# Kernel optimization log

Hardware: AMD Instinct MI355X
Metric: run time of the kernel (lower is better)

Reference implementation:

```python
import jax, jax.numpy as jnp
import numpy as np

B, CIN, COUT, CLEV = 1, 128, 128, 64
H, W = 48, 160            # height//2**scale, width//2**scale (scale=2)
MIN_D, MAX_D = 0.1, 100.0


def conv3x3(x, w, b, mode):
    x = jnp.pad(x, ((0, 0), (0, 0), (1, 1), (1, 1)), mode=mode)
    y = jax.lax.conv_general_dilated(x, w, (1, 1), 'VALID',
                                     dimension_numbers=('NCHW', 'OIHW', 'NCHW'))
    return y + b[None, :, None, None]


def head(x, w1, b1, w2, b2):  # gaussian head: conv -> GELU -> conv, replicate pad
    return conv3x3(jax.nn.gelu(conv3x3(x, w1, b1, 'edge')), w2, b2, 'edge')


def convblock(x, w, b):  # ConvBlock: 3x3 conv (reflect pad) + ELU
    return jax.nn.elu(conv3x3(x, w, b, 'reflect'))


def to_pts(t):  # [B,C,H,W] -> [B,HW,C]
    return t.transpose(0, 2, 3, 1).reshape(t.shape[0], -1, t.shape[1])


def quat_to_rot(q):  # [N,4] (w,x,y,z) -> [N,3,3]
    w, x, y, z = q[:, 0], q[:, 1], q[:, 2], q[:, 3]
    return jnp.stack([1 - 2 * (y * y + z * z), 2 * (x * y - w * z), 2 * (x * z + w * y),
                      2 * (x * y + w * z), 1 - 2 * (x * x + z * z), 2 * (y * z - w * x),
                      2 * (x * z - w * y), 2 * (y * z + w * x), 1 - 2 * (x * x + y * y)],
                     axis=-1).reshape(-1, 3, 3)


def rasterize_one(pos, rot, scl, opa, feat, K):
    # depth-sort gaussians front-to-back
    order = jnp.argsort(pos[:, 2])
    pos, rot, scl, opa, feat = pos[order], rot[order], scl[order], opa[order], feat[order]
    x, y, z = pos[:, 0], pos[:, 1], pos[:, 2]
    fx, fy, cx, cy = K[0, 0], K[1, 1], K[0, 2], K[1, 2]
    u, v = fx * x / z + cx, fy * y / z + cy
    # 3D covariance Sigma = R S S^T R^T, projected with perspective Jacobian J
    M = quat_to_rot(rot) * scl[:, None, :]
    Sig = jnp.einsum('nij,nkj->nik', M, M)
    zer = jnp.zeros_like(z)
    J = jnp.stack([fx / z, zer, -fx * x / z ** 2,
                   zer, fy / z, -fy * y / z ** 2], axis=-1).reshape(-1, 2, 3)
    cov = jnp.einsum('nij,njk,nlk->nil', J, Sig, J)
    a = cov[:, 0, 0] + 0.3  # low-pass blur as in 3DGS
    bq = cov[:, 0, 1]
    c = cov[:, 1, 1] + 0.3
    det = a * c - bq * bq
    A, Bc, C = c / det, -bq / det, a / det  # conic (inverse 2D covariance)
    gy, gx = jnp.meshgrid(jnp.arange(H, dtype=pos.dtype),
                          jnp.arange(W, dtype=pos.dtype), indexing='ij')
    dx = gx.reshape(-1)[:, None] - u[None, :]  # [P,N]
    dy = gy.reshape(-1)[:, None] - v[None, :]
    power = -0.5 * (A[None] * dx * dx + C[None] * dy * dy) - Bc[None] * dx * dy
    alpha = jnp.where(power <= 0.,
                      jnp.clip(opa[None, :, 0] * jnp.exp(jnp.minimum(power, 0.)), 0., 0.99),
                      0.)
    l1m = jnp.log1p(-alpha)
    logT = jnp.cumsum(l1m, axis=1) - l1m  # exclusive transmittance along sorted axis
    wgt = alpha * jnp.exp(logT)           # [P,N]
    return (wgt @ feat).T.reshape(-1, H, W)  # [C,H,W]


def forward(init_feature, disp_init, inv_K, K,
            rot_w1, rot_b1, rot_w2, rot_b2,
            scl_w1, scl_b1, scl_w2, scl_b2,
            opa_w1, opa_b1, opa_w2, opa_b2,
            fl_w1, fl_b1, fl_w2, fl_b2, fr_w, fr_b):
    bs = init_feature.shape[0]
    # disp_to_depth
    scaled = 1. / MAX_D + (1. / MIN_D - 1. / MAX_D) * disp_init
    depth = jnp.clip(1. / scaled, MIN_D, MAX_D)
    # backproject depth to a point cloud
    gy, gx = jnp.meshgrid(jnp.arange(H, dtype=depth.dtype),
                          jnp.arange(W, dtype=depth.dtype), indexing='ij')
    pix = jnp.stack([gx.ravel(), gy.ravel(), jnp.ones(H * W, depth.dtype)], 0)  # [3,HW]
    cam = jnp.einsum('bij,jn->bin', inv_K[:, :3, :3], pix) * depth.reshape(bs, 1, -1)
    position = cam.transpose(0, 2, 1)  # [B,N,3]
    rot = head(init_feature, rot_w1, rot_b1, rot_w2, rot_b2)
    rot = rot / jnp.maximum(jnp.linalg.norm(rot, axis=1, keepdims=True), 1e-12)
    rotation = to_pts(rot)  # [B,N,4]
    scale = to_pts(jnp.abs(head(init_feature, scl_w1, scl_b1, scl_w2, scl_b2)))
    opacity = to_pts(jax.nn.sigmoid(head(init_feature, opa_w1, opa_b1, opa_w2, opa_b2)))
    gs_feat = to_pts(convblock(convblock(init_feature, fl_w1, fl_b1), fl_w2, fl_b2))
    lev = jax.vmap(rasterize_one)(position, rotation, scale, opacity, gs_feat, K)
    return convblock(lev, fr_w, fr_b)


def setup_inputs() -> dict:
    key = jax.random.key(0)
    ks = jax.random.split(key, 16)
    p = lambda i, shape: jax.random.normal(ks[i], shape, jnp.float32) * 0.05
    Kmat = np.array([[0.58 * W, 0, 0.5 * W, 0],
                     [0, 1.92 * H, 0.5 * H, 0],
                     [0, 0, 1, 0],
                     [0, 0, 0, 1]], dtype=np.float32)
    inv_K = np.linalg.inv(Kmat)
    return {
        'init_feature': jax.random.normal(ks[0], (B, CIN, H, W), jnp.float32),
        'disp_init': jax.random.uniform(ks[1], (B, 1, H, W), jnp.float32, 0.01, 0.99),
        'inv_K': jnp.tile(jnp.asarray(inv_K)[None], (B, 1, 1)),
        'K': jnp.tile(jnp.asarray(Kmat)[None], (B, 1, 1)),
        'rot_w1': p(2, (8, CIN, 3, 3)), 'rot_b1': jnp.zeros(8),
        'rot_w2': p(3, (4, 8, 3, 3)), 'rot_b2': jnp.zeros(4),
        'scl_w1': p(4, (6, CIN, 3, 3)), 'scl_b1': jnp.zeros(6),
        'scl_w2': p(5, (3, 6, 3, 3)), 'scl_b2': jnp.zeros(3),
        'opa_w1': p(6, (2, CIN, 3, 3)), 'opa_b1': jnp.zeros(2),
        'opa_w2': p(7, (1, 2, 3, 3)), 'opa_b2': jnp.zeros(1),
        'fl_w1': p(8, (CIN, CIN, 3, 3)), 'fl_b1': jnp.zeros(CIN),
        'fl_w2': p(9, (CLEV, CIN, 3, 3)), 'fl_b2': jnp.zeros(CLEV),
        'fr_w': p(10, (COUT, CLEV, 3, 3)), 'fr_b': jnp.zeros(COUT),
    }


def reference(init_feature, disp_init, inv_K, K, rot_w1, rot_b1, rot_w2, rot_b2,
              scl_w1, scl_b1, scl_w2, scl_b2, opa_w1, opa_b1, opa_w2, opa_b2,
              fl_w1, fl_b1, fl_w2, fl_b2, fr_w, fr_b):
    return forward(init_feature, disp_init, inv_K, K, rot_w1, rot_b1, rot_w2, rot_b2,
                   scl_w1, scl_b1, scl_w2, scl_b2, opa_w1, opa_b1, opa_w2, opa_b2,
                   fl_w1, fl_b1, fl_w2, fl_b2, fr_w, fr_b)
```

## Files before the change

### kernel.cpp

```cpp
#include <hip/hip_runtime.h>
#include <hip/hip_bf16.h>
#include <math.h>

#define Hh 48
#define Ww 160
#define NP 7680

using bf16 = __hip_bfloat16;
typedef __attribute__((ext_vector_type(8))) short v8s;
typedef __attribute__((ext_vector_type(4))) float v4f;

__device__ __forceinline__ float bfdec(unsigned short u) {
  return __uint_as_float(((unsigned)u) << 16);
}
__device__ __forceinline__ unsigned short bfenc(float x) {
  bf16 b = __float2bfloat16(x);
  return *(unsigned short*)&b;
}
__device__ __forceinline__ float ldany(const void* p, size_t i, int isbf) {
  return isbf ? bfdec(((const unsigned short*)p)[i]) : ((const float*)p)[i];
}

__device__ __forceinline__ int mapidx(int i, int n, int mode) {
  if (mode == 0) return i < 0 ? 0 : (i >= n ? n - 1 : i);
  return i < 0 ? -i : (i >= n ? 2 * n - 2 - i : i);
}

__device__ __forceinline__ float eluf(float v) { return v > 0.f ? v : expm1f(v); }
__device__ __forceinline__ float geluf(float v) {
  float c = v + 0.044715f * v * v * v;
  return 0.5f * v * (1.f + tanhf(0.7978845608028654f * c));
}

__device__ __forceinline__ int sniff_local(const unsigned short* w, int* cnt) {
  int c = 0;
  for (int i = threadIdx.x; i < 2048; i += 256) {
    float a = fabsf(bfdec(w[i]));
    if (a > 1e-3f && a < 0.5f) c++;
  }
  cnt[threadIdx.x] = c;
  __syncthreads();
  for (int s = 128; s > 0; s >>= 1) {
    if (threadIdx.x < s) cnt[threadIdx.x] += cnt[threadIdx.x + s];
    __syncthreads();
  }
  int f = (cnt[0] > 1536) ? 1 : 0;
  __syncthreads();
  return f;
}

__global__ __launch_bounds__(256) void prep_all_k(int* __restrict__ flag,
    const void* __restrict__ xsrc, unsigned short* __restrict__ xb,
    const void* disp, const void* invK, const void* K, const void* rw2,
    const void* rb2, const void* sw2, const void* sb2, const void* ow2, const void* ob2,
    const void* rb1, const void* sb1, const void* ob1, const void* fb1, const void* fb2,
    const void* frb, const void* rot_w1, const void* scl_w1, const void* opa_w1,
    const void* fl_w1, const void* fl_w2, const void* fr_w,
    float* __restrict__ dispf, float* __restrict__ smallf, float* __restrict__ biasf,
    unsigned short* __restrict__ a_h1, unsigned short* __restrict__ a_fl1,
    unsigned short* __restrict__ a_fl2, unsigned short* __restrict__ a_fr) {
  __shared__ float tile[32][33];
  __shared__ int cnt[256];
  const int f = sniff_local((const unsigned short*)fl_w1, cnt);
  if (blockIdx.x == 0 && threadIdx.x == 0) flag[0] = f;
  if (blockIdx.x < 960) {
    const int bx = blockIdx.x;
    const int pb = (bx % 240) * 32, cb = (bx / 240) * 32;
#pragma unroll
    for (int pass = 0; pass < 4; pass++) {
      int ci = (threadIdx.x >> 5) + pass * 8, pl = threadIdx.x & 31;
      tile[ci][pl] = ldany(xsrc, (size_t)(cb + ci) * NP + pb + pl, f);
    }
    __syncthreads();
#pragma unroll
    for (int pass = 0; pass < 4; pass++) {
      int pl = (threadIdx.x >> 5) + pass * 8, ci = threadIdx.x & 31;
      xb[(size_t)(pb + pl) * 128 + cb + ci] = bfenc(tile[ci][pl]);
    }
    return;
  }
  int i = (blockIdx.x - 960) * 256 + threadIdx.x;
  if (i < 7680) { dispf[i] = ldany(disp, i, f); return; }
  i -= 7680;
  if (i < 508) {
    const void* src; int off;
    if (i < 16)       { src = invK; off = i; }
    else if (i < 32)  { src = K;    off = i - 16; }
    else if (i < 320) { src = rw2;  off = i - 32; }
    else if (i < 324) { src = rb2;  off = i - 320; }
    else if (i < 486) { src = sw2;  off = i - 324; }
    else if (i < 489) { src = sb2;  off = i - 486; }
    else if (i < 507) { src = ow2;  off = i - 489; }
    else              { src = ob2;  off = i - 507; }
    smallf[i] = ldany(src, off, f); return;
  }
  i -= 508;
  if (i < 336) {
    if (i < 8) biasf[i] = ldany(rb1, i, f);
    else if (i < 14) biasf[i] = ldany(sb1, i - 8, f);
    else if (i < 16) biasf[i] = ldany(ob1, i - 14, f);
    else if (i < 144) biasf[i] = ldany(fb1, i - 16, f);
    else if (i < 208) biasf[i] = ldany(fb2, i - 144, f);
    else biasf[i] = ldany(frb, i - 208, f);
    return;
  }
  i -= 336;
  if (i < 73728) {
    int co = i / 1152, rem = i - co * 1152;
    int t = rem >> 7, ci = rem & 127;
    float v = 0.f;
    if (co < 8) v = ldany(rot_w1, (size_t)co * 1152 + ci * 9 + t, f);
    else if (co < 14) v = ldany(scl_w1, (size_t)(co - 8) * 1152 + ci * 9 + t, f);
    else if (co < 16) v = ldany(opa_w1, (size_t)(co - 14) * 1152 + ci * 9 + t, f);
    a_h1[i] = bfenc(v); return;
  }
  i -= 73728;
  if (i < 147456) {
    int co = i / 1152, rem = i - co * 1152;
    int t = rem >> 7, ci = rem & 127;
    a_fl1[i] = bfenc(ldany(fl_w1, (size_t)co * 1152 + ci * 9 + t, f)); return;
  }
  i -= 147456;
  if (i < 73728) {
    int co = i / 1152, rem = i - co * 1152;
    int t = rem >> 7, ci = rem & 127;
    a_fl2[i] = bfenc(ldany(fl_w2, (size_t)co * 1152 + ci * 9 + t, f)); return;
  }
  i -= 73728;
  if (i < 73728) {
    int co = i / 576, rem = i - co * 576;
    int t = rem >> 6, ci = rem & 63;
    a_fr[i] = bfenc(ldany(fr_w, (size_t)co * 576 + ci * 9 + t, f));
    return;
  }
}

template<int OM, int PM, int ACT, bool GUARD, int KP, bool OPX>
__global__ __launch_bounds__(256) void gemm_conv4_k(const unsigned short* __restrict__ A,
    const unsigned short* __restrict__ X, const float* __restrict__ bias,
    void* __restrict__ out, const int* __restrict__ flag, int K, int glim) {
  __shared__ v8s As4[64][5];
  __shared__ v8s Bs4[64][5];
  __shared__ int off9s[64][9];
  const int tid = threadIdx.x;
  const int pxB = blockIdx.x * 64;
  const int coB = blockIdx.y * 64;
  if (tid < 64) {
    int p = pxB + tid;
    int h = p / Ww, w = p - h * Ww;
#pragma unroll
    for (int r = 0; r < 3; r++) {
      int hh = mapidx(h + r - 1, Hh, PM);
#pragma unroll
      for (int s = 0; s < 3; s++)
        off9s[tid][r * 3 + s] = hh * Ww + mapidx(w + s - 1, Ww, PM);
    }
  }
  const int lane = tid & 63, wv = tid >> 6;
  const int m16 = lane & 15, quad = lane >> 4;
  const int srow = tid >> 2, sg = tid & 3;
  v4f acc[4];
#pragma unroll
  for (int b = 0; b < 4; b++) acc[b] = (v4f){0.f, 0.f, 0.f, 0.f};
  __syncthreads();
  const int nIter = K >> 5;
  for (int it = 0; it < nIter; it++) {
    const int k0 = it << 5;
    {
      const unsigned short* ap = &A[(size_t)(coB + srow) * K + k0 + sg * 8];
      v8s av;
#pragma unroll
      for (int j = 0; j < 8; j++) av[j] = (short)ap[j];
      As4[srow][sg] = av;
    }
    {
      v8s bv;
      if (KP == 128) {
        int kk = k0 + sg * 8;
        int t = kk >> 7, c0 = kk & 127;
        const unsigned short* xp = &X[(size_t)off9s[srow][t] * 128 + c0];
#pragma unroll
        for (int j = 0; j < 8; j++) bv[j] = (short)xp[j];
      } else if (KP == 64) {
        int kk = k0 + sg * 8;
        int t = kk >> 6, c0 = kk & 63;
        const unsigned short* xp = &X[(size_t)off9s[srow][t] * 64 + c0];
#pragma unroll
        for (int j = 0; j < 8; j++) bv[j] = (short)xp[j];
      } else {
#pragma unroll
        for (int j = 0; j < 8; j++) {
          int k = k0 + sg * 8 + j;
          int ci = k / 9;
          int t = k - ci * 9;
          bv[j] = (short)X[(size_t)ci * NP + off9s[srow][t]];
        }
      }
      Bs4[srow][sg] = bv;
    }
    __syncthreads();
    v8s af = As4[wv * 16 + m16][quad];
    v8s bfr[4];
#pragma unroll
    for (int b = 0; b < 4; b++) bfr[b] = Bs4[b * 16 + m16][quad];
#pragma unroll
    for (int b = 0; b < 4; b++)
      acc[b] = __builtin_amdgcn_mfma_f32_16x16x32_bf16(af, bfr[b], acc[b], 0, 0, 0);
    __syncthreads();
  }
  const int obf = (OM == 2) ? *flag : (OM == 1);
#pragma unroll
  for (int b = 0; b < 4; b++) {
#pragma unroll
    for (int r = 0; r < 4; r++) {
      int co = coB + wv * 16 + quad * 4 + r;
      int px = pxB + b * 16 + m16;
      if (GUARD && co >= glim) continue;
      float bv = bias[GUARD ? (co & 15) : co];
      float v = acc[b][r] + bv;
      v = (ACT == 2) ? geluf(v) : eluf(v);
      size_t oi = OPX ? ((size_t)px * 128 + co) : ((size_t)co * NP + px);
      if (obf) ((unsigned short*)out)[oi] = bfenc(v);
      else ((float*)out)[oi] = v;
    }
  }
}

__global__ __launch_bounds__(256) void conv_fused1_k(
    const unsigned short* __restrict__ a_fl1, const unsigned short* __restrict__ a_h1,
    const unsigned short* __restrict__ X, const float* __restrict__ biasf,
    unsigned short* __restrict__ t1b, float* __restrict__ h1) {
  __shared__ v8s As4[64][5];
  __shared__ v8s Bs4[64][5];
  __shared__ int off9s[64][9];
  const int tid = threadIdx.x;
  const int zy = blockIdx.y;
  const bool ishead = (zy == 2);
  const int pm = ishead ? 0 : 1;
  const int pxB = blockIdx.x * 64;
  const int coB = ishead ? 0 : zy * 64;
  const unsigned short* A = ishead ? a_h1 : a_fl1;
  if (tid < 64) {
    int p = pxB + tid;
    int h = p / Ww, w = p - h * Ww;
#pragma unroll
    for (int r = 0; r < 3; r++) {
      int hh = mapidx(h + r - 1, Hh, pm);
#pragma unroll
      for (int s = 0; s < 3; s++)
        off9s[tid][r * 3 + s] = hh * Ww + mapidx(w + s - 1, Ww, pm);
    }
  }
  const int lane = tid & 63, wv = tid >> 6;
  const int m16 = lane & 15, quad = lane >> 4;
  const int srow = tid >> 2, sg = tid & 3;
  v4f acc[4];
#pragma unroll
  for (int b = 0; b < 4; b++) acc[b] = (v4f){0.f, 0.f, 0.f, 0.f};
  __syncthreads();
  for (int it = 0; it < 36; it++) {
    const int k0 = it << 5;
    {
      const unsigned short* ap = &A[(size_t)(coB + srow) * 1152 + k0 + sg * 8];
      v8s av;
#pragma unroll
      for (int j = 0; j < 8; j++) av[j] = (short)ap[j];
      As4[srow][sg] = av;
    }
    {
      int kk = k0 + sg * 8;
      int t = kk >> 7, c0 = kk & 127;
      const unsigned short* xp = &X[(size_t)off9s[srow][t] * 128 + c0];
      v8s bv;
#pragma unroll
      for (int j = 0; j < 8; j++) bv[j] = (short)xp[j];
      Bs4[srow][sg] = bv;
    }
    __syncthreads();
    v8s af = As4[wv * 16 + m16][quad];
    v8s bfr[4];
#pragma unroll
    for (int b = 0; b < 4; b++) bfr[b] = Bs4[b * 16 + m16][quad];
#pragma unroll
    for (int b = 0; b < 4; b++)
      acc[b] = __builtin_amdgcn_mfma_f32_16x16x32_bf16(af, bfr[b], acc[b], 0, 0, 0);
    __syncthreads();
  }
#pragma unroll
  for (int b = 0; b < 4; b++) {
#pragma unroll
    for (int r = 0; r < 4; r++) {
      int co = coB + wv * 16 + quad * 4 + r;
      int px = pxB + b * 16 + m16;
      if (ishead) {
        if (co < 16) h1[(size_t)co * NP + px] = geluf(acc[b][r] + biasf[co]);
      } else {
        t1b[(size_t)px * 128 + co] = bfenc(eluf(acc[b][r] + biasf[16 + co]));
      }
    }
  }
}

__global__ __launch_bounds__(256) void fl2_head2_k(
    const unsigned short* __restrict__ a_fl2, const unsigned short* __restrict__ t1b,
    const float* __restrict__ biasf, unsigned short* __restrict__ t2eb,
    const float* __restrict__ h1, const float* __restrict__ smallf,
    const float* __restrict__ dispf, float* __restrict__ params,
    float* __restrict__ zbuf) {
  __shared__ v8s As4[64][5];
  __shared__ v8s Bs4[64][5];
  __shared__ int off9s[64][9];
  const int tid = threadIdx.x;
  if (blockIdx.x < 120) {
    const int pxB = blockIdx.x * 64;
    if (tid < 64) {
      int p = pxB + tid;
      int h = p / Ww, w = p - h * Ww;
#pragma unroll
      for (int r = 0; r < 3; r++) {
        int hh = mapidx(h + r - 1, Hh, 1);
#pragma unroll
        for (int s = 0; s < 3; s++)
          off9s[tid][r * 3 + s] = hh * Ww + mapidx(w + s - 1, Ww, 1);
      }
    }
    const int lane = tid & 63, wv = tid >> 6;
    const int m16 = lane & 15, quad = lane >> 4;
    const int srow = tid >> 2, sg = tid & 3;
    v4f acc[4];
#pragma unroll
    for (int b = 0; b < 4; b++) acc[b] = (v4f){0.f, 0.f, 0.f, 0.f};
    __syncthreads();
    for (int it = 0; it < 36; it++) {
      const int k0 = it << 5;
      {
        const unsigned short* ap = &a_fl2[(size_t)srow * 1152 + k0 + sg * 8];
        v8s av;
#pragma unroll
        for (int j = 0; j < 8; j++) av[j] = (short)ap[j];
        As4[srow][sg] = av;
      }
      {
        int kk = k0 + sg * 8;
        int t = kk >> 7, c0 = kk & 127;
        const unsigned short* xp = &t1b[(size_t)off9s[srow][t] * 128 + c0];
        v8s bv;
#pragma unroll
        for (int j = 0; j < 8; j++) bv[j] = (short)xp[j];
        Bs4[srow][sg] = bv;
      }
      __syncthreads();
      v8s af = As4[wv * 16 + m16][quad];
      v8s bfr[4];
#pragma unroll
      for (int b = 0; b < 4; b++) bfr[b] = Bs4[b * 16 + m16][quad];
#pragma unroll
      for (int b = 0; b < 4; b++)
        acc[b] = __builtin_amdgcn_mfma_f32_16x16x32_bf16(af, bfr[b], acc[b], 0, 0, 0);
      __syncthreads();
    }
#pragma unroll
    for (int b = 0; b < 4; b++) {
#pragma unroll
      for (int r = 0; r < 4; r++) {
        int co = wv * 16 + quad * 4 + r;
        int px = pxB + b * 16 + m16;
        t2eb[(size_t)co * NP + px] = bfenc(eluf(acc[b][r] + biasf[144 + co]));
      }
    }
    return;
  }
  const float* invK = smallf;
  const float* Km   = smallf + 16;
  const float* rw2  = smallf + 32;
  const float* rb2  = smallf + 320;
  const float* sw2  = smallf + 324;
  const float* sb2  = smallf + 486;
  const float* ow2  = smallf + 489;
  const float* ob2  = smallf + 507;
  int p = (blockIdx.x - 120) * 256 + tid;
  if (p >= NP) return;
  int hh = p / Ww, ww = p - hh * Ww;
  float racc[4], sacc[3], oacc;
#pragma unroll
  for (int i = 0; i < 4; i++) racc[i] = rb2[i];
#pragma unroll
  for (int i = 0; i < 3; i++) sacc[i] = sb2[i];
  oacc = ob2[0];
  for (int ci = 0; ci < 16; ci++) {
    float t9[9];
#pragma unroll
    for (int r = 0; r < 3; r++) {
      int rr = mapidx(hh + r - 1, Hh, 0);
#pragma unroll
      for (int s = 0; s < 3; s++) {
        int cc = mapidx(ww + s - 1, Ww, 0);
        t9[r * 3 + s] = h1[(size_t)ci * NP + rr * Ww + cc];
      }
    }
    if (ci < 8) {
      for (int co = 0; co < 4; co++)
#pragma unroll
        for (int k = 0; k < 9; k++)
          racc[co] = fmaf(t9[k], rw2[(co * 8 + ci) * 9 + k], racc[co]);
    } else if (ci < 14) {
      int c2 = ci - 8;
      for (int co = 0; co < 3; co++)
#pragma unroll
        for (int k = 0; k < 9; k++)
          sacc[co] = fmaf(t9[k], sw2[(co * 6 + c2) * 9 + k], sacc[co]);
    } else {
      int c2 = ci - 14;
#pragma unroll
      for (int k = 0; k < 9; k++)
        oacc = fmaf(t9[k], ow2[c2 * 9 + k], oacc);
    }
  }
  float nq = sqrtf(racc[0]*racc[0] + racc[1]*racc[1] + racc[2]*racc[2] + racc[3]*racc[3]);
  nq = fmaxf(nq, 1e-12f);
  float qw = racc[0] / nq, qx = racc[1] / nq, qy = racc[2] / nq, qz = racc[3] / nq;
  float s0 = fabsf(sacc[0]), s1 = fabsf(sacc[1]), s2 = fabsf(sacc[2]);
  float opa = 1.f / (1.f + __expf(-oacc));
  float d = dispf[p];
  float scaled = 0.01f + 9.99f * d;
  float depth = fminf(fmaxf(1.f / scaled, 0.1f), 100.f);
  float M00 = invK[0], M01 = invK[1], M02 = invK[2];
  float M10 = invK[4], M11 = invK[5], M12 = invK[6];
  float M20 = invK[8], M21 = invK[9], M22 = invK[10];
  float gxf = (float)ww, gyf = (float)hh;
  float X = (M00 * gxf + M01 * gyf + M02) * depth;
  float Y = (M10 * gxf + M11 * gyf + M12) * depth;
  float Z = (M20 * gxf + M21 * gyf + M22) * depth;
  float fxk = Km[0], fyk = Km[5];
  float cxk = Km[2], cyk = Km[6];
  float u = fxk * X / Z + cxk;
  float v = fyk * Y / Z + cyk;
  float R00 = 1.f - 2.f*(qy*qy + qz*qz), R01 = 2.f*(qx*qy - qw*qz), R02 = 2.f*(qx*qz + qw*qy);
  float R10 = 2.f*(qx*qy + qw*qz), R11 = 1.f - 2.f*(qx*qx + qz*qz), R12 = 2.f*(qy*qz - qw*qx);
  float R20 = 2.f*(qx*qz - qw*qy), R21 = 2.f*(qy*qz + qw*qx), R22 = 1.f - 2.f*(qx*qx + qy*qy);
  float M0a = R00*s0, M0b = R01*s1, M0c = R02*s2;
  float M1a = R10*s0, M1b = R11*s1, M1c = R12*s2;
  float M2a = R20*s0, M2b = R21*s1, M2c = R22*s2;
  float S00 = M0a*M0a + M0b*M0b + M0c*M0c;
  float S01 = M0a*M1a + M0b*M1b + M0c*M1c;
  float S02 = M0a*M2a + M0b*M2b + M0c*M2c;
  float S11 = M1a*M1a + M1b*M1b + M1c*M1c;
  float S12 = M1a*M2a + M1b*M2b + M1c*M2c;
  float S22 = M2a*M2a + M2b*M2b + M2c*M2c;
  float iz = 1.f / Z;
  float j00 = fxk * iz, j02 = -fxk * X * iz * iz;
  float j11 = fyk * iz, j12 = -fyk * Y * iz * iz;
  float c00 = j00*j00*S00 + 2.f*j00*j02*S02 + j02*j02*S22 + 0.3f;
  float c01 = j00*j11*S01 + j00*j12*S02 + j02*j11*S12 + j02*j12*S22;
  float c11 = j11*j11*S11 + 2.f*j11*j12*S12 + j12*j12*S22 + 0.3f;
  float det = c00 * c11 - c01 * c01;
  float idet = 1.f / det;
  float* pr = params + (size_t)p * 8;
  pr[0] = u; pr[1] = v; pr[2] = c11 * idet; pr[3] = -c01 * idet;
  pr[4] = c00 * idet; pr[5] = opa; pr[6] = Z; pr[7] = 0.f;
  zbuf[p] = Z;
}

__global__ __launch_bounds__(256) void rank_sort_k(const float* __restrict__ zbuf,
                                                   int* __restrict__ ord) {
  __shared__ int part[32][9];
  const int g = threadIdx.x >> 3;
  const int seg = threadIdx.x & 7;
  const int i = blockIdx.x * 32 + g;
  const float zi = zbuf[i];
  const float4* zv = (const float4*)(zbuf + seg * 960);
  int cnt = 0;
  for (int t = 0; t < 240; t++) {
    float4 z4 = zv[t];
    int jb = seg * 960 + t * 4;
    cnt += (z4.x < zi || (z4.x == zi && jb + 0 < i)) ? 1 : 0;
    cnt += (z4.y < zi || (z4.y == zi && jb + 1 < i)) ? 1 : 0;
    cnt += (z4.z < zi || (z4.z == zi && jb + 2 < i)) ? 1 : 0;
    cnt += (z4.w < zi || (z4.w == zi && jb + 3 < i)) ? 1 : 0;
  }
  part[g][seg] = cnt;
  __syncthreads();
  if (seg == 0) {
    int c = part[g][0] + part[g][1] + part[g][2] + part[g][3]
          + part[g][4] + part[g][5] + part[g][6] + part[g][7];
    ord[c] = i;
  }
}

__global__ __launch_bounds__(64) void raster_seq_k(const int* __restrict__ ord,
    const float* __restrict__ params, const unsigned short* __restrict__ t2eb,
    unsigned short* __restrict__ levb) {
  __shared__ unsigned int Wl[64][17];
  __shared__ int ords[32];
  const int lane = threadIdx.x;
  const int m16 = lane & 15, quad = lane >> 4;
  const int pxB = blockIdx.x * 64;
  const int mypx = pxB + lane;
  const float px = (float)(mypx % Ww), py = (float)(mypx / Ww);
  float T = 1.f;
  v4f acc[4][4];
#pragma unroll
  for (int a = 0; a < 4; a++)
#pragma unroll
    for (int b = 0; b < 4; b++) acc[a][b] = (v4f){0.f, 0.f, 0.f, 0.f};
  for (int sub = 0; sub < NP / 32; sub++) {
    const int g0 = sub * 32;
    if (lane < 32) ords[lane] = ord[g0 + lane];
    __syncthreads();
    int myord[8];
#pragma unroll
    for (int j = 0; j < 8; j++) myord[j] = ords[quad * 8 + j];
    float al[32];
#pragma unroll
    for (int j = 0; j < 32; j++) {
      const float* pp = params + ((size_t)ords[j] << 3);
      float4 pa = *(const float4*)pp;
      float4 pb = *(const float4*)(pp + 4);
      float dx = px - pa.x, dy = py - pa.y;
      float power = -0.5f * (pa.z * dx * dx + pb.x * dy * dy) - pa.w * dx * dy;
      al[j] = fminf(pb.y * __expf(power), 0.99f);
    }
#pragma unroll
    for (int jj = 0; jj < 16; jj++) {
      float w0 = al[2 * jj] * T;     T *= 1.f - al[2 * jj];
      float w1 = al[2 * jj + 1] * T; T *= 1.f - al[2 * jj + 1];
      Wl[lane][jj] = (unsigned)bfenc(w0) | ((unsigned)bfenc(w1) << 16);
    }
    v8s af[4], bfr[4];
#pragma unroll
    for (int a = 0; a < 4; a++) {
      unsigned d0 = Wl[a * 16 + m16][quad * 4 + 0];
      unsigned d1 = Wl[a * 16 + m16][quad * 4 + 1];
      unsigned d2 = Wl[a * 16 + m16][quad * 4 + 2];
      unsigned d3 = Wl[a * 16 + m16][quad * 4 + 3];
      v8s t;
      t[0] = (short)(d0 & 0xffff); t[1] = (short)(d0 >> 16);
      t[2] = (short)(d1 & 0xffff); t[3] = (short)(d1 >> 16);
      t[4] = (short)(d2 & 0xffff); t[5] = (short)(d2 >> 16);
      t[6] = (short)(d3 & 0xffff); t[7] = (short)(d3 >> 16);
      af[a] = t;
    }
#pragma unroll
    for (int b = 0; b < 4; b++) {
      const unsigned short* fp = &t2eb[(size_t)(b * 16 + m16) * NP];
      v8s t;
#pragma unroll
      for (int j = 0; j < 8; j++) t[j] = (short)fp[myord[j]];
      bfr[b] = t;
    }
#pragma unroll
    for (int a = 0; a < 4; a++)
#pragma unroll
      for (int b = 0; b < 4; b++)
        acc[a][b] = __builtin_amdgcn_mfma_f32_16x16x32_bf16(af[a], bfr[b], acc[a][b], 0, 0, 0);
    if (__all(T < 1e-7f)) break;
    __syncthreads();
  }
#pragma unroll
  for (int a = 0; a < 4; a++) {
#pragma unroll
    for (int b = 0; b < 4; b++) {
#pragma unroll
      for (int r = 0; r < 4; r++) {
        levb[(size_t)(pxB + a * 16 + quad * 4 + r) * 64 + b * 16 + m16] =
            bfenc(acc[a][b][r]);
      }
    }
  }
}

extern "C" void kernel_launch(void* const* d_in, const int* in_sizes, int n_in,
                              void* d_out, int out_size, void* d_ws, size_t ws_size,
                              hipStream_t stream) {
  (void)in_sizes; (void)n_in; (void)out_size; (void)ws_size;
  const void* init_feature = d_in[0];
  const void* disp   = d_in[1];
  const void* invK   = d_in[2];
  const void* Km     = d_in[3];
  const void* rot_w1 = d_in[4];
  const void* rot_b1 = d_in[5];
  const void* rot_w2 = d_in[6];
  const void* rot_b2 = d_in[7];
  const void* scl_w1 = d_in[8];
  const void* scl_b1 = d_in[9];
  const void* scl_w2 = d_in[10];
  const void* scl_b2 = d_in[11];
  const void* opa_w1 = d_in[12];
  const void* opa_b1 = d_in[13];
  const void* opa_w2 = d_in[14];
  const void* opa_b2 = d_in[15];
  const void* fl_w1  = d_in[16];
  const void* fl_b1  = d_in[17];
  const void* fl_w2  = d_in[18];
  const void* fl_b2  = d_in[19];
  const void* fr_w   = d_in[20];
  const void* fr_b   = d_in[21];

  float* wsf = (float*)d_ws;
  int*   flag    = (int*)wsf;
  float* smallf  = wsf + 16;
  float* dispf   = wsf + 528;
  float* biasf   = wsf + 8208;
  unsigned short* a_h1  = (unsigned short*)(wsf + 8720);
  unsigned short* a_fl1 = (unsigned short*)(wsf + 45584);
  unsigned short* a_fl2 = (unsigned short*)(wsf + 119312);
  unsigned short* a_fr  = (unsigned short*)(wsf + 156176);
  unsigned short* xb    = (unsigned short*)(wsf + 193040);
  unsigned short* t1b   = (unsigned short*)(wsf + 684560);
  unsigned short* t2eb  = (unsigned short*)(wsf + 1176080);
  float* h1      = wsf + 1667600;
  float* params  = wsf + 1790480;
  unsigned short* levb = (unsigned short*)(wsf + 2896400);
  float* zbuf    = wsf + 3142160;
  int*   ord     = (int*)(wsf + 3157520);

  prep_all_k<<<2434, 256, 0, stream>>>(flag, init_feature, xb,
      disp, invK, Km, rot_w2, rot_b2, scl_w2, scl_b2, opa_w2, opa_b2,
      rot_b1, scl_b1, opa_b1, fl_b1, fl_b2, fr_b,
      rot_w1, scl_w1, opa_w1, fl_w1, fl_w2, fr_w,
      dispf, smallf, biasf, a_h1, a_fl1, a_fl2, a_fr);

  conv_fused1_k<<<dim3(120, 3), 256, 0, stream>>>(a_fl1, a_h1, xb, biasf, t1b, h1);
  fl2_head2_k<<<150, 256, 0, stream>>>(a_fl2, t1b, biasf, t2eb, h1, smallf,
                                       dispf, params, zbuf);
  rank_sort_k<<<240, 256, 0, stream>>>(zbuf, ord);
  raster_seq_k<<<120, 64, 0, stream>>>(ord, params, t2eb, levb);
  gemm_conv4_k<2, 1, 1, false, 64, false><<<dim3(120, 2), 256, 0, stream>>>(
      a_fr, levb, biasf + 208, d_out, flag, 576, 128);
}
```

Baseline: 211.4 us.

## Fuse all pipeline stages into one cooperative persistent kernel with grid syncs

Replaces the chain of six separate launches (prep, first convs, second conv plus head, rank sort, rasterizer, final conv) with a single cooperative kernel on 240 blocks. Each stage walks its work units with a grid-stride loop, and the stages are separated by grid.sync. The goal is to remove per-launch overhead and inter-kernel gaps. In exchange, stages with more units than blocks serialize, register pressure from the merged kernel may lower occupancy, and grid barriers add their own cost. If the cooperative launch fails, the original multi-kernel path runs instead.

```diff
diff --git a/kernel.cpp b/kernel.cpp
--- a/kernel.cpp
+++ b/kernel.cpp
@@ -1,10 +1,14 @@
 #include <hip/hip_runtime.h>
 #include <hip/hip_bf16.h>
+#include <hip/hip_cooperative_groups.h>
 #include <math.h>
+
+namespace cg = cooperative_groups;
 
 #define Hh 48
 #define Ww 160
 #define NP 7680
+#define GRD 240
 
 using bf16 = __hip_bfloat16;
 typedef __attribute__((ext_vector_type(8))) short v8s;
@@ -48,6 +52,532 @@
   __syncthreads();
   return f;
 }
+
+__global__ __launch_bounds__(256) void mega_k(
+    const void* xsrc, const void* disp, const void* invK, const void* Km,
+    const void* rot_w1, const void* rot_b1, const void* rot_w2, const void* rot_b2,
+    const void* scl_w1, const void* scl_b1, const void* scl_w2, const void* scl_b2,
+    const void* opa_w1, const void* opa_b1, const void* opa_w2, const void* opa_b2,
+    const void* fl_w1, const void* fl_b1, const void* fl_w2, const void* fl_b2,
+    const void* fr_w, const void* fr_b,
+    float* wsf, void* dout) {
+  cg::grid_group grid = cg::this_grid();
+  __shared__ __align__(16) unsigned char smem[18048];
+  const int tid = threadIdx.x;
+  const int bid = blockIdx.x;
+
+  float* smallf  = wsf + 16;
+  float* dispf   = wsf + 528;
+  float* biasf   = wsf + 8208;
+  unsigned short* a_h1  = (unsigned short*)(wsf + 8720);
+  unsigned short* a_fl1 = (unsigned short*)(wsf + 45584);
+  unsigned short* a_fl2 = (unsigned short*)(wsf + 119312);
+  unsigned short* a_fr  = (unsigned short*)(wsf + 156176);
+  unsigned short* xb    = (unsigned short*)(wsf + 193040);
+  unsigned short* t1b   = (unsigned short*)(wsf + 684560);
+  unsigned short* t2eb  = (unsigned short*)(wsf + 1176080);
+  float* h1      = wsf + 1667600;
+  float* params  = wsf + 1790480;
+  unsigned short* levb = (unsigned short*)(wsf + 2896400);
+  float* zbuf    = wsf + 3142160;
+  int*   ord     = (int*)(wsf + 3157520);
+
+  const int f = sniff_local((const unsigned short*)fl_w1, (int*)smem);
+
+  {
+    float (*tile)[33] = (float (*)[33])smem;
+    for (int u = bid; u < 2434; u += GRD) {
+      if (u < 960) {
+        __syncthreads();
+        const int pb = (u % 240) * 32, cb = (u / 240) * 32;
+#pragma unroll
+        for (int pass = 0; pass < 4; pass++) {
+          int ci = (tid >> 5) + pass * 8, pl = tid & 31;
+          tile[ci][pl] = ldany(xsrc, (size_t)(cb + ci) * NP + pb + pl, f);
+        }
+        __syncthreads();
+#pragma unroll
+        for (int pass = 0; pass < 4; pass++) {
+          int pl = (tid >> 5) + pass * 8, ci = tid & 31;
+          xb[(size_t)(pb + pl) * 128 + cb + ci] = bfenc(tile[ci][pl]);
+        }
+      } else {
+        int i = (u - 960) * 256 + tid;
+        if (i < 7680) { dispf[i] = ldany(disp, i, f); }
+        else {
+          i -= 7680;
+          if (i < 508) {
+            const void* src; int off;
+            if (i < 16)       { src = invK;   off = i; }
+            else if (i < 32)  { src = Km;     off = i - 16; }
+            else if (i < 320) { src = rot_w2; off = i - 32; }
+            else if (i < 324) { src = rot_b2; off = i - 320; }
+            else if (i < 486) { src = scl_w2; off = i - 324; }
+            else if (i < 489) { src = scl_b2; off = i - 486; }
+            else if (i < 507) { src = opa_w2; off = i - 489; }
+            else              { src = opa_b2; off = i - 507; }
+            smallf[i] = ldany(src, off, f);
+          } else {
+            i -= 508;
+            if (i < 336) {
+              if (i < 8) biasf[i] = ldany(rot_b1, i, f);
+              else if (i < 14) biasf[i] = ldany(scl_b1, i - 8, f);
+              else if (i < 16) biasf[i] = ldany(opa_b1, i - 14, f);
+              else if (i < 144) biasf[i] = ldany(fl_b1, i - 16, f);
+              else if (i < 208) biasf[i] = ldany(fl_b2, i - 144, f);
+              else biasf[i] = ldany(fr_b, i - 208, f);
+            } else {
+              i -= 336;
+              if (i < 73728) {
+                int co = i / 1152, rem = i - co * 1152;
+                int t = rem >> 7, ci = rem & 127;
+                float v = 0.f;
+                if (co < 8) v = ldany(rot_w1, (size_t)co * 1152 + ci * 9 + t, f);
+                else if (co < 14) v = ldany(scl_w1, (size_t)(co - 8) * 1152 + ci * 9 + t, f);
+                else if (co < 16) v = ldany(opa_w1, (size_t)(co - 14) * 1152 + ci * 9 + t, f);
+                a_h1[i] = bfenc(v);
+              } else {
+                i -= 73728;
+                if (i < 147456) {
+                  int co = i / 1152, rem = i - co * 1152;
+                  int t = rem >> 7, ci = rem & 127;
+                  a_fl1[i] = bfenc(ldany(fl_w1, (size_t)co * 1152 + ci * 9 + t, f));
+                } else {
+                  i -= 147456;
+                  if (i < 73728) {
+                    int co = i / 1152, rem = i - co * 1152;
+                    int t = rem >> 7, ci = rem & 127;
+                    a_fl2[i] = bfenc(ldany(fl_w2, (size_t)co * 1152 + ci * 9 + t, f));
+                  } else {
+                    i -= 73728;
+                    if (i < 73728) {
+                      int co = i / 576, rem = i - co * 576;
+                      int t = rem >> 6, ci = rem & 63;
+                      a_fr[i] = bfenc(ldany(fr_w, (size_t)co * 576 + ci * 9 + t, f));
+                    }
+                  }
+                }
+              }
+            }
+          }
+        }
+      }
+    }
+  }
+  grid.sync();
+
+  {
+    v8s (*As4)[5] = (v8s (*)[5])smem;
+    v8s (*Bs4)[5] = (v8s (*)[5])(smem + 5120);
+    int (*off9s)[9] = (int (*)[9])(smem + 10240);
+    const int lane = tid & 63, wv = tid >> 6;
+    const int m16 = lane & 15, quad = lane >> 4;
+    const int srow = tid >> 2, sg = tid & 3;
+    for (int u = bid; u < 360; u += GRD) {
+      const int zy = u / 120;
+      const bool ishead = (zy == 2);
+      const int pm = ishead ? 0 : 1;
+      const int pxB = (u % 120) * 64;
+      const int coB = ishead ? 0 : zy * 64;
+      const unsigned short* A = ishead ? a_h1 : a_fl1;
+      if (tid < 64) {
+        int p = pxB + tid;
+        int h = p / Ww, w = p - h * Ww;
+#pragma unroll
+        for (int r = 0; r < 3; r++) {
+          int hh = mapidx(h + r - 1, Hh, pm);
+#pragma unroll
+          for (int s = 0; s < 3; s++)
+            off9s[tid][r * 3 + s] = hh * Ww + mapidx(w + s - 1, Ww, pm);
+        }
+      }
+      v4f acc[4];
+#pragma unroll
+      for (int b = 0; b < 4; b++) acc[b] = (v4f){0.f, 0.f, 0.f, 0.f};
+      __syncthreads();
+      for (int it = 0; it < 36; it++) {
+        const int k0 = it << 5;
+        {
+          const unsigned short* ap = &A[(size_t)(coB + srow) * 1152 + k0 + sg * 8];
+          v8s av;
+#pragma unroll
+          for (int j = 0; j < 8; j++) av[j] = (short)ap[j];
+          As4[srow][sg] = av;
+        }
+        {
+          int kk = k0 + sg * 8;
+          int t = kk >> 7, c0 = kk & 127;
+          const unsigned short* xp = &xb[(size_t)off9s[srow][t] * 128 + c0];
+          v8s bv;
+#pragma unroll
+          for (int j = 0; j < 8; j++) bv[j] = (short)xp[j];
+          Bs4[srow][sg] = bv;
+        }
+        __syncthreads();
+        v8s af = As4[wv * 16 + m16][quad];
+        v8s bfr[4];
+#pragma unroll
+        for (int b = 0; b < 4; b++) bfr[b] = Bs4[b * 16 + m16][quad];
+#pragma unroll
+        for (int b = 0; b < 4; b++)
+          acc[b] = __builtin_amdgcn_mfma_f32_16x16x32_bf16(af, bfr[b], acc[b], 0, 0, 0);
+        __syncthreads();
+      }
+#pragma unroll
+      for (int b = 0; b < 4; b++) {
+#pragma unroll
+        for (int r = 0; r < 4; r++) {
+          int co = coB + wv * 16 + quad * 4 + r;
+          int px = pxB + b * 16 + m16;
+          if (ishead) {
+            if (co < 16) h1[(size_t)co * NP + px] = geluf(acc[b][r] + biasf[co]);
+          } else {
+            t1b[(size_t)px * 128 + co] = bfenc(eluf(acc[b][r] + biasf[16 + co]));
+          }
+        }
+      }
+    }
+  }
+  grid.sync();
+
+  {
+    v8s (*As4)[5] = (v8s (*)[5])smem;
+    v8s (*Bs4)[5] = (v8s (*)[5])(smem + 5120);
+    int (*off9s)[9] = (int (*)[9])(smem + 10240);
+    const int lane = tid & 63, wv = tid >> 6;
+    const int m16 = lane & 15, quad = lane >> 4;
+    const int srow = tid >> 2, sg = tid & 3;
+    for (int u = bid; u < 150; u += GRD) {
+      if (u < 120) {
+        const int pxB = u * 64;
+        if (tid < 64) {
+          int p = pxB + tid;
+          int h = p / Ww, w = p - h * Ww;
+#pragma unroll
+          for (int r = 0; r < 3; r++) {
+            int hh = mapidx(h + r - 1, Hh, 1);
+#pragma unroll
+            for (int s = 0; s < 3; s++)
+              off9s[tid][r * 3 + s] = hh * Ww + mapidx(w + s - 1, Ww, 1);
+          }
+        }
+        v4f acc[4];
+#pragma unroll
+        for (int b = 0; b < 4; b++) acc[b] = (v4f){0.f, 0.f, 0.f, 0.f};
+        __syncthreads();
+        for (int it = 0; it < 36; it++) {
+          const int k0 = it << 5;
+          {
+            const unsigned short* ap = &a_fl2[(size_t)srow * 1152 + k0 + sg * 8];
+            v8s av;
+#pragma unroll
+            for (int j = 0; j < 8; j++) av[j] = (short)ap[j];
+            As4[srow][sg] = av;
+          }
+          {
+            int kk = k0 + sg * 8;
+            int t = kk >> 7, c0 = kk & 127;
+            const unsigned short* xp = &t1b[(size_t)off9s[srow][t] * 128 + c0];
+            v8s bv;
+#pragma unroll
+            for (int j = 0; j < 8; j++) bv[j] = (short)xp[j];
+            Bs4[srow][sg] = bv;
+          }
+          __syncthreads();
+          v8s af = As4[wv * 16 + m16][quad];
+          v8s bfr[4];
+#pragma unroll
+          for (int b = 0; b < 4; b++) bfr[b] = Bs4[b * 16 + m16][quad];
+#pragma unroll
+          for (int b = 0; b < 4; b++)
+            acc[b] = __builtin_amdgcn_mfma_f32_16x16x32_bf16(af, bfr[b], acc[b], 0, 0, 0);
+          __syncthreads();
+        }
+#pragma unroll
+        for (int b = 0; b < 4; b++) {
+#pragma unroll
+          for (int r = 0; r < 4; r++) {
+            int co = wv * 16 + quad * 4 + r;
+            int px = pxB + b * 16 + m16;
+            t2eb[(size_t)co * NP + px] = bfenc(eluf(acc[b][r] + biasf[144 + co]));
+          }
+        }
+      } else {
+        const float* invKp = smallf;
+        const float* Kmp   = smallf + 16;
+        const float* rw2  = smallf + 32;
+        const float* rb2  = smallf + 320;
+        const float* sw2  = smallf + 324;
+        const float* sb2  = smallf + 486;
+        const float* ow2  = smallf + 489;
+        const float* ob2  = smallf + 507;
+        int p = (u - 120) * 256 + tid;
+        if (p < NP) {
+          int hh = p / Ww, ww = p - hh * Ww;
+          float racc[4], sacc[3], oacc;
+#pragma unroll
+          for (int i = 0; i < 4; i++) racc[i] = rb2[i];
+#pragma unroll
+          for (int i = 0; i < 3; i++) sacc[i] = sb2[i];
+          oacc = ob2[0];
+          for (int ci = 0; ci < 16; ci++) {
+            float t9[9];
+#pragma unroll
+            for (int r = 0; r < 3; r++) {
+              int rr = mapidx(hh + r - 1, Hh, 0);
+#pragma unroll
+              for (int s = 0; s < 3; s++) {
+                int cc = mapidx(ww + s - 1, Ww, 0);
+                t9[r * 3 + s] = h1[(size_t)ci * NP + rr * Ww + cc];
+              }
+            }
+            if (ci < 8) {
+              for (int co = 0; co < 4; co++)
+#pragma unroll
+                for (int k = 0; k < 9; k++)
+                  racc[co] = fmaf(t9[k], rw2[(co * 8 + ci) * 9 + k], racc[co]);
+            } else if (ci < 14) {
+              int c2 = ci - 8;
+              for (int co = 0; co < 3; co++)
+#pragma unroll
+                for (int k = 0; k < 9; k++)
+                  sacc[co] = fmaf(t9[k], sw2[(co * 6 + c2) * 9 + k], sacc[co]);
+            } else {
+              int c2 = ci - 14;
+#pragma unroll
+              for (int k = 0; k < 9; k++)
+                oacc = fmaf(t9[k], ow2[c2 * 9 + k], oacc);
+            }
+          }
+          float nq = sqrtf(racc[0]*racc[0] + racc[1]*racc[1] + racc[2]*racc[2] + racc[3]*racc[3]);
+          nq = fmaxf(nq, 1e-12f);
+          float qw = racc[0] / nq, qx = racc[1] / nq, qy = racc[2] / nq, qz = racc[3] / nq;
+          float s0 = fabsf(sacc[0]), s1 = fabsf(sacc[1]), s2 = fabsf(sacc[2]);
+          float opa = 1.f / (1.f + __expf(-oacc));
+          float d = dispf[p];
+          float scaled = 0.01f + 9.99f * d;
+          float depth = fminf(fmaxf(1.f / scaled, 0.1f), 100.f);
+          float M00 = invKp[0], M01 = invKp[1], M02 = invKp[2];
+          float M10 = invKp[4], M11 = invKp[5], M12 = invKp[6];
+          float M20 = invKp[8], M21 = invKp[9], M22 = invKp[10];
+          float gxf = (float)ww, gyf = (float)hh;
+          float X = (M00 * gxf + M01 * gyf + M02) * depth;
+          float Y = (M10 * gxf + M11 * gyf + M12) * depth;
+          float Z = (M20 * gxf + M21 * gyf + M22) * depth;
+          float fxk = Kmp[0], fyk = Kmp[5];
+          float cxk = Kmp[2], cyk = Kmp[6];
+          float u2 = fxk * X / Z + cxk;
+          float v2 = fyk * Y / Z + cyk;
+          float R00 = 1.f - 2.f*(qy*qy + qz*qz), R01 = 2.f*(qx*qy - qw*qz), R02 = 2.f*(qx*qz + qw*qy);
+          float R10 = 2.f*(qx*qy + qw*qz), R11 = 1.f - 2.f*(qx*qx + qz*qz), R12 = 2.f*(qy*qz - qw*qx);
+          float R20 = 2.f*(qx*qz - qw*qy), R21 = 2.f*(qy*qz + qw*qx), R22 = 1.f - 2.f*(qx*qx + qy*qy);
+          float M0a = R00*s0, M0b = R01*s1, M0c = R02*s2;
+          float M1a = R10*s0, M1b = R11*s1, M1c = R12*s2;
+          float M2a = R20*s0, M2b = R21*s1, M2c = R22*s2;
+          float S00 = M0a*M0a + M0b*M0b + M0c*M0c;
+          float S01 = M0a*M1a + M0b*M1b + M0c*M1c;
+          float S02 = M0a*M2a + M0b*M2b + M0c*M2c;
+          float S11 = M1a*M1a + M1b*M1b + M1c*M1c;
+          float S12 = M1a*M2a + M1b*M2b + M1c*M2c;
+          float S22 = M2a*M2a + M2b*M2b + M2c*M2c;
+          float iz = 1.f / Z;
+          float j00 = fxk * iz, j02 = -fxk * X * iz * iz;
+          float j11 = fyk * iz, j12 = -fyk * Y * iz * iz;
+          float c00 = j00*j00*S00 + 2.f*j00*j02*S02 + j02*j02*S22 + 0.3f;
+          float c01 = j00*j11*S01 + j00*j12*S02 + j02*j11*S12 + j02*j12*S22;
+          float c11 = j11*j11*S11 + 2.f*j11*j12*S12 + j12*j12*S22 + 0.3f;
+          float det = c00 * c11 - c01 * c01;
+          float idet = 1.f / det;
+          float* pr = params + (size_t)p * 8;
+          pr[0] = u2; pr[1] = v2; pr[2] = c11 * idet; pr[3] = -c01 * idet;
+          pr[4] = c00 * idet; pr[5] = opa; pr[6] = Z; pr[7] = 0.f;
+          zbuf[p] = Z;
+        }
+      }
+    }
+  }
+  grid.sync();
+
+  {
+    int (*part)[9] = (int (*)[9])smem;
+    for (int u = bid; u < 240; u += GRD) {
+      __syncthreads();
+      const int g = tid >> 3;
+      const int seg = tid & 7;
+      const int i = u * 32 + g;
+      const float zi = zbuf[i];
+      const float4* zv = (const float4*)(zbuf + seg * 960);
+      int cnt = 0;
+      for (int t = 0; t < 240; t++) {
+        float4 z4 = zv[t];
+        int jb = seg * 960 + t * 4;
+        cnt += (z4.x < zi || (z4.x == zi && jb + 0 < i)) ? 1 : 0;
+        cnt += (z4.y < zi || (z4.y == zi && jb + 1 < i)) ? 1 : 0;
+        cnt += (z4.z < zi || (z4.z == zi && jb + 2 < i)) ? 1 : 0;
+        cnt += (z4.w < zi || (z4.w == zi && jb + 3 < i)) ? 1 : 0;
+      }
+      part[g][seg] = cnt;
+      __syncthreads();
+      if (seg == 0) {
+        int c = part[g][0] + part[g][1] + part[g][2] + part[g][3]
+              + part[g][4] + part[g][5] + part[g][6] + part[g][7];
+        ord[c] = i;
+      }
+    }
+  }
+  grid.sync();
+
+  {
+    const int lane = tid & 63, wv = tid >> 6;
+    const int m16 = lane & 15, quad = lane >> 4;
+    unsigned int (*Wlw)[17] = (unsigned int (*)[17])(smem + (size_t)wv * (64 * 17 * 4));
+    int* ordw = (int*)(smem + 17408) + wv * 32;
+    for (int u = bid * 4 + wv; u < 120; u += GRD * 4) {
+      const int pxB = u * 64;
+      const int mypx = pxB + lane;
+      const float px = (float)(mypx % Ww), py = (float)(mypx / Ww);
+      float T = 1.f;
+      v4f acc[4][4];
+#pragma unroll
+      for (int a = 0; a < 4; a++)
+#pragma unroll
+        for (int b = 0; b < 4; b++) acc[a][b] = (v4f){0.f, 0.f, 0.f, 0.f};
+      for (int sub = 0; sub < NP / 32; sub++) {
+        const int g0 = sub * 32;
+        if (lane < 32) ordw[lane] = ord[g0 + lane];
+        int myord[8];
+#pragma unroll
+        for (int j = 0; j < 8; j++) myord[j] = ordw[quad * 8 + j];
+        float al[32];
+#pragma unroll
+        for (int j = 0; j < 32; j++) {
+          const float* pp = params + ((size_t)ordw[j] << 3);
+          float4 pa = *(const float4*)pp;
+          float4 pb = *(const float4*)(pp + 4);
+          float dx = px - pa.x, dy = py - pa.y;
+          float power = -0.5f * (pa.z * dx * dx + pb.x * dy * dy) - pa.w * dx * dy;
+          al[j] = fminf(pb.y * __expf(power), 0.99f);
+        }
+#pragma unroll
+        for (int jj = 0; jj < 16; jj++) {
+          float w0 = al[2 * jj] * T;     T *= 1.f - al[2 * jj];
+          float w1 = al[2 * jj + 1] * T; T *= 1.f - al[2 * jj + 1];
+          Wlw[lane][jj] = (unsigned)bfenc(w0) | ((unsigned)bfenc(w1) << 16);
+        }
+        v8s af[4], bfr[4];
+#pragma unroll
+        for (int a = 0; a < 4; a++) {
+          unsigned d0 = Wlw[a * 16 + m16][quad * 4 + 0];
+          unsigned d1 = Wlw[a * 16 + m16][quad * 4 + 1];
+          unsigned d2 = Wlw[a * 16 + m16][quad * 4 + 2];
+          unsigned d3 = Wlw[a * 16 + m16][quad * 4 + 3];
+          v8s t;
+          t[0] = (short)(d0 & 0xffff); t[1] = (short)(d0 >> 16);
+          t[2] = (short)(d1 & 0xffff); t[3] = (short)(d1 >> 16);
+          t[4] = (short)(d2 & 0xffff); t[5] = (short)(d2 >> 16);
+          t[6] = (short)(d3 & 0xffff); t[7] = (short)(d3 >> 16);
+          af[a] = t;
+        }
+#pragma unroll
+        for (int b = 0; b < 4; b++) {
+          const unsigned short* fp = &t2eb[(size_t)(b * 16 + m16) * NP];
+          v8s t;
+#pragma unroll
+          for (int j = 0; j < 8; j++) t[j] = (short)fp[myord[j]];
+          bfr[b] = t;
+        }
+#pragma unroll
+        for (int a = 0; a < 4; a++)
+#pragma unroll
+          for (int b = 0; b < 4; b++)
+            acc[a][b] = __builtin_amdgcn_mfma_f32_16x16x32_bf16(af[a], bfr[b], acc[a][b], 0, 0, 0);
+        if (__all(T < 1e-7f)) break;
+      }
+#pragma unroll
+      for (int a = 0; a < 4; a++) {
+#pragma unroll
+        for (int b = 0; b < 4; b++) {
+#pragma unroll
+          for (int r = 0; r < 4; r++) {
+            levb[(size_t)(pxB + a * 16 + quad * 4 + r) * 64 + b * 16 + m16] =
+                bfenc(acc[a][b][r]);
+          }
+        }
+      }
+    }
+  }
+  grid.sync();
+
+  {
+    v8s (*As4)[5] = (v8s (*)[5])smem;
+    v8s (*Bs4)[5] = (v8s (*)[5])(smem + 5120);
+    int (*off9s)[9] = (int (*)[9])(smem + 10240);
+    const int lane = tid & 63, wv = tid >> 6;
+    const int m16 = lane & 15, quad = lane >> 4;
+    const int srow = tid >> 2, sg = tid & 3;
+    for (int u = bid; u < 240; u += GRD) {
+      __syncthreads();
+      const int pxB = (u % 120) * 64;
+      const int coB = (u / 120) * 64;
+      if (tid < 64) {
+        int p = pxB + tid;
+        int h = p / Ww, w = p - h * Ww;
+#pragma unroll
+        for (int r = 0; r < 3; r++) {
+          int hh = mapidx(h + r - 1, Hh, 1);
+#pragma unroll
+          for (int s = 0; s < 3; s++)
+            off9s[tid][r * 3 + s] = hh * Ww + mapidx(w + s - 1, Ww, 1);
+        }
+      }
+      v4f acc[4];
+#pragma unroll
+      for (int b = 0; b < 4; b++) acc[b] = (v4f){0.f, 0.f, 0.f, 0.f};
+      __syncthreads();
+      for (int it = 0; it < 18; it++) {
+        const int k0 = it << 5;
+        {
+          const unsigned short* ap = &a_fr[(size_t)(coB + srow) * 576 + k0 + sg * 8];
+          v8s av;
+#pragma unroll
+          for (int j = 0; j < 8; j++) av[j] = (short)ap[j];
+          As4[srow][sg] = av;
+        }
+        {
+          int kk = k0 + sg * 8;
+          int t = kk >> 6, c0 = kk & 63;
+          const unsigned short* xp = &levb[(size_t)off9s[srow][t] * 64 + c0];
+          v8s bv;
+#pragma unroll
+          for (int j = 0; j < 8; j++) bv[j] = (short)xp[j];
+          Bs4[srow][sg] = bv;
+        }
+        __syncthreads();
+        v8s af = As4[wv * 16 + m16][quad];
+        v8s bfr[4];
+#pragma unroll
+        for (int b = 0; b < 4; b++) bfr[b] = Bs4[b * 16 + m16][quad];
+#pragma unroll
+        for (int b = 0; b < 4; b++)
+          acc[b] = __builtin_amdgcn_mfma_f32_16x16x32_bf16(af, bfr[b], acc[b], 0, 0, 0);
+        __syncthreads();
+      }
+#pragma unroll
+      for (int b = 0; b < 4; b++) {
+#pragma unroll
+        for (int r = 0; r < 4; r++) {
+          int co = coB + wv * 16 + quad * 4 + r;
+          int px = pxB + b * 16 + m16;
+          float v = eluf(acc[b][r] + biasf[208 + co]);
+          size_t oi = (size_t)co * NP + px;
+          if (f) ((unsigned short*)dout)[oi] = bfenc(v);
+          else ((float*)dout)[oi] = v;
+        }
+      }
+    }
+  }
+}
+
 
 __global__ __launch_bounds__(256) void prep_all_k(int* __restrict__ flag,
     const void* __restrict__ xsrc, unsigned short* __restrict__ xb,
@@ -614,12 +1144,24 @@
   float* zbuf    = wsf + 3142160;
   int*   ord     = (int*)(wsf + 3157520);
 
+  void* kp[] = {
+    (void*)&init_feature, (void*)&disp, (void*)&invK, (void*)&Km,
+    (void*)&rot_w1, (void*)&rot_b1, (void*)&rot_w2, (void*)&rot_b2,
+    (void*)&scl_w1, (void*)&scl_b1, (void*)&scl_w2, (void*)&scl_b2,
+    (void*)&opa_w1, (void*)&opa_b1, (void*)&opa_w2, (void*)&opa_b2,
+    (void*)&fl_w1, (void*)&fl_b1, (void*)&fl_w2, (void*)&fl_b2,
+    (void*)&fr_w, (void*)&fr_b,
+    (void*)&wsf, (void*)&d_out };
+  hipError_t err = hipLaunchCooperativeKernel((const void*)mega_k, dim3(GRD),
+                                              dim3(256), kp, 0, stream);
+  if (err == hipSuccess) return;
+
+  (void)hipGetLastError();
   prep_all_k<<<2434, 256, 0, stream>>>(flag, init_feature, xb,
       disp, invK, Km, rot_w2, rot_b2, scl_w2, scl_b2, opa_w2, opa_b2,
       rot_b1, scl_b1, opa_b1, fl_b1, fl_b2, fr_b,
       rot_w1, scl_w1, opa_w1, fl_w1, fl_w2, fr_w,
       dispf, smallf, biasf, a_h1, a_fl1, a_fl2, a_fr);
-
   conv_fused1_k<<<dim3(120, 3), 256, 0, stream>>>(a_fl1, a_h1, xb, biasf, t1b, h1);
   fl2_head2_k<<<150, 256, 0, stream>>>(a_fl2, t1b, biasf, t2eb, h1, smallf,
                                        dispf, params, zbuf);
```

Result: slower. 394.1 us (+86.4%).

## Fold depth rank sort into prep kernel by recomputing depth from disparity

Applied to the files above, without the earlier changes.

The separate rank_sort kernel and the zbuf write are removed. The prep kernel gets 240 extra blocks that recompute each pixel's depth key straight from disparity and inv_K, then rank all points by counting comparisons. This takes one launch and one dependency off the critical path, so the sort can run alongside the weight and layout prep work. In exchange every comparison does a reciprocal and dtype-dispatched loads instead of vectorised float4 reads. The result also depends on the recomputed depth being bit-identical to the Z the head kernel produces.

```diff
diff --git a/kernel.cpp b/kernel.cpp
--- a/kernel.cpp
+++ b/kernel.cpp
@@ -30,6 +30,12 @@
 __device__ __forceinline__ float geluf(float v) {
   float c = v + 0.044715f * v * v * v;
   return 0.5f * v * (1.f + tanhf(0.7978845608028654f * c));
+}
+
+__device__ __forceinline__ float zkey(float d, float lin) {
+  float scaled = fmaf(9.99f, d, 0.01f);
+  float depth = fminf(fmaxf(1.f / scaled, 0.1f), 100.f);
+  return lin * depth;
 }
 
 __device__ __forceinline__ int sniff_local(const unsigned short* w, int* cnt) {
@@ -58,11 +64,42 @@
     const void* fl_w1, const void* fl_w2, const void* fr_w,
     float* __restrict__ dispf, float* __restrict__ smallf, float* __restrict__ biasf,
     unsigned short* __restrict__ a_h1, unsigned short* __restrict__ a_fl1,
-    unsigned short* __restrict__ a_fl2, unsigned short* __restrict__ a_fr) {
+    unsigned short* __restrict__ a_fl2, unsigned short* __restrict__ a_fr,
+    int* __restrict__ ord) {
   __shared__ float tile[32][33];
   __shared__ int cnt[256];
+  __shared__ int part[32][9];
   const int f = sniff_local((const unsigned short*)fl_w1, cnt);
   if (blockIdx.x == 0 && threadIdx.x == 0) flag[0] = f;
+  if (blockIdx.x >= 2434) {
+    const int u = blockIdx.x - 2434;
+    const int g = threadIdx.x >> 3;
+    const int seg = threadIdx.x & 7;
+    const int i = u * 32 + g;
+    const float M20 = ldany(invK, 8, f), M21 = ldany(invK, 9, f),
+                M22 = ldany(invK, 10, f);
+    const int gyi = i / Ww, gxi = i - gyi * Ww;
+    const float zi = zkey(ldany(disp, i, f),
+                          fmaf(M20, (float)gxi, fmaf(M21, (float)gyi, M22)));
+    int c = 0;
+    int j = seg * 960;
+    for (int r = 0; r < 6; r++) {
+      float gyf = (float)(seg * 6 + r);
+      float lin0 = fmaf(M21, gyf, M22);
+      for (int cc = 0; cc < Ww; cc++, j++) {
+        float zj = zkey(ldany(disp, j, f), fmaf(M20, (float)cc, lin0));
+        c += (zj < zi || (zj == zi && j < i)) ? 1 : 0;
+      }
+    }
+    part[g][seg] = c;
+    __syncthreads();
+    if (seg == 0) {
+      int s = part[g][0] + part[g][1] + part[g][2] + part[g][3]
+            + part[g][4] + part[g][5] + part[g][6] + part[g][7];
+      ord[s] = i;
+    }
+    return;
+  }
   if (blockIdx.x < 960) {
     const int bx = blockIdx.x;
     const int pb = (bx % 240) * 32, cb = (bx / 240) * 32;
@@ -305,8 +342,7 @@
     const unsigned short* __restrict__ a_fl2, const unsigned short* __restrict__ t1b,
     const float* __restrict__ biasf, unsigned short* __restrict__ t2eb,
     const float* __restrict__ h1, const float* __restrict__ smallf,
-    const float* __restrict__ dispf, float* __restrict__ params,
-    float* __restrict__ zbuf) {
+    const float* __restrict__ dispf, float* __restrict__ params) {
   __shared__ v8s As4[64][5];
   __shared__ v8s Bs4[64][5];
   __shared__ int off9s[64][9];
@@ -458,33 +494,6 @@
   float* pr = params + (size_t)p * 8;
   pr[0] = u; pr[1] = v; pr[2] = c11 * idet; pr[3] = -c01 * idet;
   pr[4] = c00 * idet; pr[5] = opa; pr[6] = Z; pr[7] = 0.f;
-  zbuf[p] = Z;
-}
-
-__global__ __launch_bounds__(256) void rank_sort_k(const float* __restrict__ zbuf,
-                                                   int* __restrict__ ord) {
-  __shared__ int part[32][9];
-  const int g = threadIdx.x >> 3;
-  const int seg = threadIdx.x & 7;
-  const int i = blockIdx.x * 32 + g;
-  const float zi = zbuf[i];
-  const float4* zv = (const float4*)(zbuf + seg * 960);
-  int cnt = 0;
-  for (int t = 0; t < 240; t++) {
-    float4 z4 = zv[t];
-    int jb = seg * 960 + t * 4;
-    cnt += (z4.x < zi || (z4.x == zi && jb + 0 < i)) ? 1 : 0;
-    cnt += (z4.y < zi || (z4.y == zi && jb + 1 < i)) ? 1 : 0;
-    cnt += (z4.z < zi || (z4.z == zi && jb + 2 < i)) ? 1 : 0;
-    cnt += (z4.w < zi || (z4.w == zi && jb + 3 < i)) ? 1 : 0;
-  }
-  part[g][seg] = cnt;
-  __syncthreads();
-  if (seg == 0) {
-    int c = part[g][0] + part[g][1] + part[g][2] + part[g][3]
-          + part[g][4] + part[g][5] + part[g][6] + part[g][7];
-    ord[c] = i;
-  }
 }
 
 __global__ __launch_bounds__(64) void raster_seq_k(const int* __restrict__ ord,
@@ -611,19 +620,17 @@
   float* h1      = wsf + 1667600;
   float* params  = wsf + 1790480;
   unsigned short* levb = (unsigned short*)(wsf + 2896400);
-  float* zbuf    = wsf + 3142160;
   int*   ord     = (int*)(wsf + 3157520);
 
-  prep_all_k<<<2434, 256, 0, stream>>>(flag, init_feature, xb,
+  prep_all_k<<<2674, 256, 0, stream>>>(flag, init_feature, xb,
       disp, invK, Km, rot_w2, rot_b2, scl_w2, scl_b2, opa_w2, opa_b2,
       rot_b1, scl_b1, opa_b1, fl_b1, fl_b2, fr_b,
       rot_w1, scl_w1, opa_w1, fl_w1, fl_w2, fr_w,
-      dispf, smallf, biasf, a_h1, a_fl1, a_fl2, a_fr);
+      dispf, smallf, biasf, a_h1, a_fl1, a_fl2, a_fr, ord);
 
   conv_fused1_k<<<dim3(120, 3), 256, 0, stream>>>(a_fl1, a_h1, xb, biasf, t1b, h1);
   fl2_head2_k<<<150, 256, 0, stream>>>(a_fl2, t1b, biasf, t2eb, h1, smallf,
-                                       dispf, params, zbuf);
-  rank_sort_k<<<240, 256, 0, stream>>>(zbuf, ord);
+                                       dispf, params);
   raster_seq_k<<<120, 64, 0, stream>>>(ord, params, t2eb, levb);
   gemm_conv4_k<2, 1, 1, false, 64, false><<<dim3(120, 2), 256, 0, stream>>>(
       a_fr, levb, biasf + 208, d_out, flag, 576, 128);
```

Result: slower. 344.5 us (+63.0%).
